# Kernel optimization log

Hardware: AMD Instinct MI355X
Metric: run time of the kernel (lower is better)

Reference implementation:

```python
import jax, jax.numpy as jnp
import numpy as np

INPUT_SIZE = 4
SEQ = 256
EMB = 64
QKV = 64
BATCH = 64
INDICES = np.array([0, 0, 1, 1])
BLK = SEQ // INPUT_SIZE                      # 64 positions per block
POS_GROUP = np.repeat(INDICES, BLK)          # per-position group id, shape [SEQ]
NUM_HEADS = len(np.unique(INDICES))          # 2
GROUP_POS = [np.where(POS_GROUP == g)[0] for g in range(NUM_HEADS)]  # static index sets


def _linear_params(key, din, dout):
    # torch nn.Linear default init: U(-1/sqrt(din), 1/sqrt(din))
    kw, kb = jax.random.split(key)
    s = 1.0 / np.sqrt(din)
    W = jax.random.uniform(kw, (dout, din), jnp.float32, -s, s)
    b = jax.random.uniform(kb, (dout,), jnp.float32, -s, s)
    return W, b


def setup_inputs() -> dict:
    key = jax.random.key(0)
    keys = jax.random.split(key, 1 + 3 * NUM_HEADS)
    inp = {"x": jax.random.normal(keys[0], (BATCH, SEQ, EMB), jnp.float32)}
    for g in range(NUM_HEADS):
        L = len(GROUP_POS[g])                # 128
        din, dout = L * EMB, L * QKV         # 8192 -> 8192
        WQ, bQ = _linear_params(keys[1 + 3 * g + 0], din, dout)
        WK, bK = _linear_params(keys[1 + 3 * g + 1], din, dout)
        WV, bV = _linear_params(keys[1 + 3 * g + 2], din, dout)
        inp[f"WQ{g}"], inp[f"bQ{g}"] = WQ, bQ
        inp[f"WK{g}"], inp[f"bK{g}"] = WK, bK
        inp[f"WV{g}"], inp[f"bV{g}"] = WV, bV
    return inp


def _head(xs, WQ, bQ, WK, bK, WV, bV, L):
    # xs: [B, L*EMB] flattened group slice
    B = xs.shape[0]
    Q = (xs @ WQ.T + bQ).reshape(B, L, QKV)
    K = (xs @ WK.T + bK).reshape(B, L, QKV)
    V = (xs @ WV.T + bV).reshape(B, L, QKV)
    scores = jnp.einsum("bik,bjk->bij", Q, K)        # [B, L, L]
    # Original uses nn.Softmax(dim=1): normalize over the QUERY axis (axis=1).
    attn = jax.nn.softmax(scores, axis=1)
    Z = jnp.einsum("bij,bjk->bik", attn, V)
    # coeff applied AFTER attention @ V, as in the original
    return Z * (1.0 / jnp.sqrt(jnp.float32(QKV)))


def reference(x, WQ0, bQ0, WK0, bK0, WV0, bV0, WQ1, bQ1, WK1, bK1, WV1, bV1):
    params = [(WQ0, bQ0, WK0, bK0, WV0, bV0), (WQ1, bQ1, WK1, bK1, WV1, bV1)]
    B = x.shape[0]
    out = jnp.zeros((B, SEQ, QKV), jnp.float32)
    for g in range(NUM_HEADS):                        # small static loop over groups
        pos = GROUP_POS[g]
        L = len(pos)
        xs = x[:, pos, :].reshape(B, L * EMB)
        Z = _head(xs, *params[g], L)
        out = out.at[:, pos, :].set(Z)
    return out
```

## Files before the change

### kernel.cpp

```cpp
#include <hip/hip_runtime.h>
#include <hip/hip_bf16.h>

#define BATCH 64
#define SEQ   256
#define EMB   64
#define QKVD  64
#define KD    8192
#define ND    8192
#define SEQD  16384
#define BKT   256
#define NTK   (KD / BKT)

typedef __attribute__((ext_vector_type(8))) short bf16x8;
typedef __attribute__((ext_vector_type(4))) float f32x4;

struct WArgs { const float* W[6]; const float* b[6]; };

__device__ __forceinline__ short f2bf(float f) {
    unsigned u = __builtin_bit_cast(unsigned, f);
    u += 0x7fffu + ((u >> 16) & 1u);
    return (short)(u >> 16);
}

__device__ __forceinline__ void gl16(const void* g, void* l) {
    __builtin_amdgcn_global_load_lds(
        (const __attribute__((address_space(1))) void*)g,
        (__attribute__((address_space(3))) void*)l, 16, 0, 0);
}

__device__ __forceinline__ void barrier_fenced() {
    asm volatile("" ::: "memory");
    __builtin_amdgcn_s_barrier();
    asm volatile("" ::: "memory");
}

__global__ __launch_bounds__(256)
void cvt_x_kernel(const float* __restrict__ x, short* __restrict__ xb) {
    const int i = (blockIdx.x * 256 + threadIdx.x) * 4;
    float4 v = *reinterpret_cast<const float4*>(x + i);
    short4 o;
    o.x = f2bf(v.x); o.y = f2bf(v.y); o.z = f2bf(v.z); o.w = f2bf(v.w);
    *reinterpret_cast<short4*>(xb + i) = o;
}

__global__ __launch_bounds__(256, 1)
void qkv_gemm_kernel(const short* __restrict__ xb, WArgs wa,
                     float* __restrict__ qkv) {
    __shared__ __attribute__((aligned(16))) float W_lds[2][64 * BKT];
    __shared__ __attribute__((aligned(16))) short A_lds[64 * BKT];

    const int wv = threadIdx.x >> 6;
    const int ln = threadIdx.x & 63;
    const int r  = ln & 15;
    const int kb = ln >> 4;
    const int key = r & 7;

    for (int nt = 0; nt < 3; ++nt) {
        const int logical = blockIdx.x * 3 + nt;
        const int gi = logical >> 7;
        const int n0 = (logical & 127) * 64;
        const int g  = gi / 3;

        const char*  __restrict__ Wb8 =
            (const char*)(wa.W[gi] + (size_t)(n0 + wv * 16) * KD);
        const short* __restrict__ Ag = xb + g * KD;

        f32x4 acc0 = {0.f, 0.f, 0.f, 0.f};
        f32x4 acc1 = acc0, acc2 = acc0, acc3 = acc0;

        auto stageW = [&](int t, int slot) {
            const char* tb = Wb8 + (size_t)t * 1024;
            #pragma unroll
            for (int i = 0; i < 16; ++i) {
                gl16(tb + (size_t)i * (KD * 4) + ((ln ^ (i & 7)) << 4),
                     (char*)&W_lds[slot][0] + (wv * 16 + i) * 1024);
            }
        };
        auto stageA = [&](int t) {
            #pragma unroll
            for (int j = 0; j < 8; ++j) {
                const int jj  = wv * 8 + j;
                const int row = 2 * jj + (ln >> 5);
                const int c   = (ln & 31) ^ (row & 7);
                gl16((const char*)(Ag + (size_t)row * SEQD) + (size_t)t * 512 + (c << 4),
                     (char*)&A_lds[0] + jj * 1024);
            }
        };

        auto compute = [&](int slot) {
            const float* Wrow = &W_lds[slot][0] + (wv * 16 + r) * BKT;
            const char*  Ab   = (const char*)&A_lds[0];
            #pragma unroll
            for (int s = 0; s < 8; ++s) {
                const int cg = s * 8 + kb * 2;
                f32x4 w0 = *(const f32x4*)(Wrow + (((cg)     ^ key) << 2));
                f32x4 w1 = *(const f32x4*)(Wrow + (((cg + 1) ^ key) << 2));
                bf16x8 bb;
                bb[0] = f2bf(w0[0]); bb[1] = f2bf(w0[1]);
                bb[2] = f2bf(w0[2]); bb[3] = f2bf(w0[3]);
                bb[4] = f2bf(w1[0]); bb[5] = f2bf(w1[1]);
                bb[6] = f2bf(w1[2]); bb[7] = f2bf(w1[3]);
                const int ca = (s * 4 + kb) ^ key;
                const bf16x8 a0 = *(const bf16x8*)(Ab + (r)      * 512 + (ca << 4));
                const bf16x8 a1 = *(const bf16x8*)(Ab + (r + 16) * 512 + (ca << 4));
                const bf16x8 a2 = *(const bf16x8*)(Ab + (r + 32) * 512 + (ca << 4));
                const bf16x8 a3 = *(const bf16x8*)(Ab + (r + 48) * 512 + (ca << 4));
                acc0 = __builtin_amdgcn_mfma_f32_16x16x32_bf16(a0, bb, acc0, 0, 0, 0);
                acc1 = __builtin_amdgcn_mfma_f32_16x16x32_bf16(a1, bb, acc1, 0, 0, 0);
                acc2 = __builtin_amdgcn_mfma_f32_16x16x32_bf16(a2, bb, acc2, 0, 0, 0);
                acc3 = __builtin_amdgcn_mfma_f32_16x16x32_bf16(a3, bb, acc3, 0, 0, 0);
            }
        };

        stageW(0, 0);
        stageA(0);
        stageW(1, 1);

        for (int t = 0; t < NTK; ++t) {
            if (t < NTK - 2) { asm volatile("s_waitcnt vmcnt(16)" ::: "memory"); }
            else             { asm volatile("s_waitcnt vmcnt(0)"  ::: "memory"); }
            __builtin_amdgcn_sched_barrier(0);
            barrier_fenced();
            compute(t & 1);
            barrier_fenced();
            if (t + 1 < NTK) stageA(t + 1);
            if (t + 2 < NTK) stageW(t + 2, t & 1);
        }
        barrier_fenced();

        const int nbr = n0 + wv * 16 + r;
        const float bias = wa.b[gi][nbr];
        float* orow = qkv + (size_t)gi * (BATCH * ND) + nbr;
        #pragma unroll
        for (int reg = 0; reg < 4; ++reg) {
            const int m = kb * 4 + reg;
            orow[(size_t)(m)      * ND] = acc0[reg] + bias;
            orow[(size_t)(m + 16) * ND] = acc1[reg] + bias;
            orow[(size_t)(m + 32) * ND] = acc2[reg] + bias;
            orow[(size_t)(m + 48) * ND] = acc3[reg] + bias;
        }
    }
}

__global__ __launch_bounds__(256)
void attn_kernel(const float* __restrict__ qkv, float* __restrict__ out) {
    __shared__ float Ql[128 * 65];
    __shared__ float Kl[128 * 65];
    __shared__ float Sc[128 * 129];
    __shared__ float Pm[256];
    __shared__ float Ps[256];
    __shared__ float Rden[128];

    const int b = blockIdx.x;
    const int g = blockIdx.y;
    const int t = threadIdx.x;

    const float* __restrict__ Qg = qkv + ((size_t)(3 * g + 0) * BATCH + b) * ND;
    const float* __restrict__ Kg = qkv + ((size_t)(3 * g + 1) * BATCH + b) * ND;
    const float* __restrict__ Vg = qkv + ((size_t)(3 * g + 2) * BATCH + b) * ND;

    for (int e = t; e < 8192; e += 256) {
        const int i = e >> 6, k = e & 63;
        Ql[i * 65 + k] = Qg[e];
        Kl[i * 65 + k] = Kg[e];
    }
    __syncthreads();

    {
        const int i0 = (t >> 4) * 8;
        const int j0 = (t & 15) * 8;
        float s[8][8];
        #pragma unroll
        for (int rr = 0; rr < 8; ++rr)
            #pragma unroll
            for (int cc = 0; cc < 8; ++cc) s[rr][cc] = 0.f;
        for (int k = 0; k < 64; ++k) {
            float qv[8], kv[8];
            #pragma unroll
            for (int rr = 0; rr < 8; ++rr) qv[rr] = Ql[(i0 + rr) * 65 + k];
            #pragma unroll
            for (int cc = 0; cc < 8; ++cc) kv[cc] = Kl[(j0 + cc) * 65 + k];
            #pragma unroll
            for (int rr = 0; rr < 8; ++rr)
                #pragma unroll
                for (int cc = 0; cc < 8; ++cc)
                    s[rr][cc] = fmaf(qv[rr], kv[cc], s[rr][cc]);
        }
        #pragma unroll
        for (int rr = 0; rr < 8; ++rr)
            #pragma unroll
            for (int cc = 0; cc < 8; ++cc)
                Sc[(i0 + rr) * 129 + (j0 + cc)] = s[rr][cc];
    }
    __syncthreads();

    const int j = t & 127, h = t >> 7;
    {
        for (int e = t; e < 8192; e += 256) {
            const int i = e >> 6, k = e & 63;
            Ql[i * 65 + k] = Vg[e];
        }
        float m = -3.0e38f;
        for (int i = h * 64; i < h * 64 + 64; ++i)
            m = fmaxf(m, Sc[i * 129 + j]);
        Pm[h * 128 + j] = m;
    }
    __syncthreads();
    {
        const float m = fmaxf(Pm[j], Pm[128 + j]);
        float sum = 0.f;
        for (int i = h * 64; i < h * 64 + 64; ++i) {
            const float e = __expf(Sc[i * 129 + j] - m);
            Sc[i * 129 + j] = e;
            sum += e;
        }
        Ps[h * 128 + j] = sum;
    }
    __syncthreads();
    if (t < 128) Rden[t] = 1.0f / (Ps[t] + Ps[128 + t]);
    __syncthreads();

    {
        const int i0 = (t >> 4) * 8;
        const int k0 = (t & 15) * 4;
        float z[8][4];
        #pragma unroll
        for (int rr = 0; rr < 8; ++rr)
            #pragma unroll
            for (int cc = 0; cc < 4; ++cc) z[rr][cc] = 0.f;
        for (int jj = 0; jj < 128; ++jj) {
            const float rd = Rden[jj];
            float av[8], vv[4];
            #pragma unroll
            for (int rr = 0; rr < 8; ++rr) av[rr] = Sc[(i0 + rr) * 129 + jj] * rd;
            #pragma unroll
            for (int cc = 0; cc < 4; ++cc) vv[cc] = Ql[jj * 65 + k0 + cc];
            #pragma unroll
            for (int rr = 0; rr < 8; ++rr)
                #pragma unroll
                for (int cc = 0; cc < 4; ++cc)
                    z[rr][cc] = fmaf(av[rr], vv[cc], z[rr][cc]);
        }
        float* op = out + (size_t)b * (SEQ * QKVD) + (size_t)(g * 128) * QKVD + k0;
        #pragma unroll
        for (int rr = 0; rr < 8; ++rr) {
            float4 o;
            o.x = z[rr][0] * 0.125f; o.y = z[rr][1] * 0.125f;
            o.z = z[rr][2] * 0.125f; o.w = z[rr][3] * 0.125f;
            *reinterpret_cast<float4*>(op + (size_t)(i0 + rr) * QKVD) = o;
        }
    }
}

extern "C" void kernel_launch(void* const* d_in, const int* in_sizes, int n_in,
                              void* d_out, int out_size, void* d_ws, size_t ws_size,
                              hipStream_t stream) {
    const float* x = (const float*)d_in[0];
    WArgs wa;
    for (int g = 0; g < 2; ++g)
        for (int q = 0; q < 3; ++q) {
            wa.W[g * 3 + q] = (const float*)d_in[1 + g * 6 + q * 2];
            wa.b[g * 3 + q] = (const float*)d_in[2 + g * 6 + q * 2];
        }

    short* xb  = (short*)d_ws;
    float* qkv = (float*)((char*)d_ws + (size_t)4 * 1024 * 1024);

    cvt_x_kernel<<<dim3(1024), dim3(256), 0, stream>>>(x, xb);
    qkv_gemm_kernel<<<dim3(256), dim3(256), 0, stream>>>(xb, wa, qkv);
    attn_kernel<<<dim3(BATCH, 2), dim3(256), 0, stream>>>(qkv, (float*)d_out);
}
```

Before: 345.0 us.

## Retile QKV GEMM to 32-column tiles with finer K pipelining and XCD-aware mapping

The QKV GEMM changes from 256 persistent blocks, each looping over three 64-column tiles, to 1536 blocks that each own one 32-column tile. Each wave now computes half the batch rows, with a deeper pipeline that double-buffers 512-wide W chunks and 128-wide A chunks. A block-index remap interleaves blocks across the 8 XCDs. The goal is better occupancy and overlap of the weight stream. The cost is that A is reloaded more often per weight byte, and the vmcnt bookkeeping is more complex.

New measurement: 515.9 us. 49.6% more time.

```diff
diff --git a/kernel.cpp b/kernel.cpp
--- a/kernel.cpp
+++ b/kernel.cpp
@@ -8,8 +8,10 @@
 #define KD    8192
 #define ND    8192
 #define SEQD  16384
-#define BKT   256
-#define NTK   (KD / BKT)
+#define BKP   512
+#define BKH2  128
+#define NPAIR (KD / BKP)
+#define NHALF (KD / BKH2)
 
 typedef __attribute__((ext_vector_type(8))) short bf16x8;
 typedef __attribute__((ext_vector_type(4))) float f32x4;
@@ -46,99 +48,127 @@
 __global__ __launch_bounds__(256, 1)
 void qkv_gemm_kernel(const short* __restrict__ xb, WArgs wa,
                      float* __restrict__ qkv) {
-    __shared__ __attribute__((aligned(16))) float W_lds[2][64 * BKT];
-    __shared__ __attribute__((aligned(16))) short A_lds[64 * BKT];
+    __shared__ __attribute__((aligned(16))) float W_lds[2][2][16 * BKP];
+    __shared__ __attribute__((aligned(16))) short A_lds[2][64 * BKH2];
 
     const int wv = threadIdx.x >> 6;
     const int ln = threadIdx.x & 63;
     const int r  = ln & 15;
     const int kb = ln >> 4;
-    const int key = r & 7;
-
-    for (int nt = 0; nt < 3; ++nt) {
-        const int logical = blockIdx.x * 3 + nt;
-        const int gi = logical >> 7;
-        const int n0 = (logical & 127) * 64;
-        const int g  = gi / 3;
-
-        const char*  __restrict__ Wb8 =
-            (const char*)(wa.W[gi] + (size_t)(n0 + wv * 16) * KD);
-        const short* __restrict__ Ag = xb + g * KD;
-
-        f32x4 acc0 = {0.f, 0.f, 0.f, 0.f};
-        f32x4 acc1 = acc0, acc2 = acc0, acc3 = acc0;
-
-        auto stageW = [&](int t, int slot) {
-            const char* tb = Wb8 + (size_t)t * 1024;
-            #pragma unroll
-            for (int i = 0; i < 16; ++i) {
-                gl16(tb + (size_t)i * (KD * 4) + ((ln ^ (i & 7)) << 4),
-                     (char*)&W_lds[slot][0] + (wv * 16 + i) * 1024);
+    const int gr = wv >> 1;
+    const int mh = wv & 1;
+
+    const int bid     = blockIdx.x;
+    const int logical = (bid & 7) * 192 + (bid >> 3);
+    const int gi      = logical >> 8;
+    const int n0      = (logical & 255) * 32;
+    const int g       = gi / 3;
+
+    const char*  __restrict__ Wgrp =
+        (const char*)(wa.W[gi] + (size_t)(n0 + gr * 16) * KD);
+    const short* __restrict__ Ag = xb + g * KD;
+
+    f32x4 acc0 = {0.f, 0.f, 0.f, 0.f};
+    f32x4 acc1 = acc0;
+
+    auto stageW = [&](int p, int slot) {
+        const char* pb = Wgrp + (size_t)p * 2048;
+        #pragma unroll
+        for (int i = 0; i < 8; ++i) {
+            const int row = mh * 8 + i;
+            const char* rp = pb + (size_t)row * (KD * 4);
+            char* ld = (char*)&W_lds[gr][slot][0] + row * 2048;
+            #pragma unroll
+            for (int j = 0; j < 2; ++j) {
+                const int sc = (j * 64 + ln) ^ (row & 7);
+                gl16(rp + sc * 16, ld + j * 1024 + ln * 16);
             }
-        };
-        auto stageA = [&](int t) {
-            #pragma unroll
-            for (int j = 0; j < 8; ++j) {
-                const int jj  = wv * 8 + j;
-                const int row = 2 * jj + (ln >> 5);
-                const int c   = (ln & 31) ^ (row & 7);
-                gl16((const char*)(Ag + (size_t)row * SEQD) + (size_t)t * 512 + (c << 4),
-                     (char*)&A_lds[0] + jj * 1024);
-            }
-        };
-
-        auto compute = [&](int slot) {
-            const float* Wrow = &W_lds[slot][0] + (wv * 16 + r) * BKT;
-            const char*  Ab   = (const char*)&A_lds[0];
-            #pragma unroll
-            for (int s = 0; s < 8; ++s) {
-                const int cg = s * 8 + kb * 2;
-                f32x4 w0 = *(const f32x4*)(Wrow + (((cg)     ^ key) << 2));
-                f32x4 w1 = *(const f32x4*)(Wrow + (((cg + 1) ^ key) << 2));
-                bf16x8 bb;
-                bb[0] = f2bf(w0[0]); bb[1] = f2bf(w0[1]);
-                bb[2] = f2bf(w0[2]); bb[3] = f2bf(w0[3]);
-                bb[4] = f2bf(w1[0]); bb[5] = f2bf(w1[1]);
-                bb[6] = f2bf(w1[2]); bb[7] = f2bf(w1[3]);
-                const int ca = (s * 4 + kb) ^ key;
-                const bf16x8 a0 = *(const bf16x8*)(Ab + (r)      * 512 + (ca << 4));
-                const bf16x8 a1 = *(const bf16x8*)(Ab + (r + 16) * 512 + (ca << 4));
-                const bf16x8 a2 = *(const bf16x8*)(Ab + (r + 32) * 512 + (ca << 4));
-                const bf16x8 a3 = *(const bf16x8*)(Ab + (r + 48) * 512 + (ca << 4));
-                acc0 = __builtin_amdgcn_mfma_f32_16x16x32_bf16(a0, bb, acc0, 0, 0, 0);
-                acc1 = __builtin_amdgcn_mfma_f32_16x16x32_bf16(a1, bb, acc1, 0, 0, 0);
-                acc2 = __builtin_amdgcn_mfma_f32_16x16x32_bf16(a2, bb, acc2, 0, 0, 0);
-                acc3 = __builtin_amdgcn_mfma_f32_16x16x32_bf16(a3, bb, acc3, 0, 0, 0);
-            }
-        };
-
-        stageW(0, 0);
-        stageA(0);
-        stageW(1, 1);
-
-        for (int t = 0; t < NTK; ++t) {
-            if (t < NTK - 2) { asm volatile("s_waitcnt vmcnt(16)" ::: "memory"); }
-            else             { asm volatile("s_waitcnt vmcnt(0)"  ::: "memory"); }
-            __builtin_amdgcn_sched_barrier(0);
-            barrier_fenced();
-            compute(t & 1);
-            barrier_fenced();
-            if (t + 1 < NTK) stageA(t + 1);
-            if (t + 2 < NTK) stageW(t + 2, t & 1);
-        }
-        barrier_fenced();
-
-        const int nbr = n0 + wv * 16 + r;
-        const float bias = wa.b[gi][nbr];
-        float* orow = qkv + (size_t)gi * (BATCH * ND) + nbr;
-        #pragma unroll
-        for (int reg = 0; reg < 4; ++reg) {
-            const int m = kb * 4 + reg;
-            orow[(size_t)(m)      * ND] = acc0[reg] + bias;
-            orow[(size_t)(m + 16) * ND] = acc1[reg] + bias;
-            orow[(size_t)(m + 32) * ND] = acc2[reg] + bias;
-            orow[(size_t)(m + 48) * ND] = acc3[reg] + bias;
-        }
+        }
+    };
+
+    auto stageA = [&](int h) {
+        short* slot = &A_lds[h & 1][0];
+        const char* hb = (const char*)Ag + (size_t)h * 256;
+        #pragma unroll
+        for (int ii = 0; ii < 4; ++ii) {
+            const int row = wv * 16 + ii * 4 + (ln >> 4);
+            const int sc  = (ln & 15) ^ ((row & 7) << 1);
+            gl16(hb + (size_t)row * (SEQD * 2) + sc * 16,
+                 (char*)slot + (wv * 4 + ii) * 1024 + ln * 16);
+        }
+    };
+
+    auto compute = [&](int h) {
+        const float* Wrow = &W_lds[gr][(h >> 2) & 1][0] + r * BKP;
+        const char*  Ab   = (const char*)&A_lds[h & 1][0];
+        const int    key  = r & 7;
+        #pragma unroll
+        for (int s = 0; s < 4; ++s) {
+            const int lg = (h & 3) * 32 + s * 8 + kb * 2;
+            f32x4 w0 = *(const f32x4*)(Wrow + (((lg)     ^ key) << 2));
+            f32x4 w1 = *(const f32x4*)(Wrow + (((lg + 1) ^ key) << 2));
+            bf16x8 bb;
+            bb[0] = f2bf(w0[0]); bb[1] = f2bf(w0[1]);
+            bb[2] = f2bf(w0[2]); bb[3] = f2bf(w0[3]);
+            bb[4] = f2bf(w1[0]); bb[5] = f2bf(w1[1]);
+            bb[6] = f2bf(w1[2]); bb[7] = f2bf(w1[3]);
+            const int ca = ((s * 4 + kb) ^ (key << 1)) << 4;
+            const bf16x8 a0 = *(const bf16x8*)(Ab + (mh * 32 + r)      * 256 + ca);
+            const bf16x8 a1 = *(const bf16x8*)(Ab + (mh * 32 + 16 + r) * 256 + ca);
+            acc0 = __builtin_amdgcn_mfma_f32_16x16x32_bf16(a0, bb, acc0, 0, 0, 0);
+            acc1 = __builtin_amdgcn_mfma_f32_16x16x32_bf16(a1, bb, acc1, 0, 0, 0);
+        }
+    };
+
+    stageW(0, 0);
+    stageA(0);
+    stageA(1);
+    __builtin_amdgcn_sched_barrier(0);
+
+    for (int p = 0; p < NPAIR; ++p) {
+        const int h = 4 * p;
+        const bool morew = (p + 1 < NPAIR);
+
+        asm volatile("s_waitcnt vmcnt(4)" ::: "memory");
+        barrier_fenced();
+        compute(h);
+        barrier_fenced();
+        stageA(h + 2);
+        __builtin_amdgcn_sched_barrier(0);
+
+        asm volatile("s_waitcnt vmcnt(4)" ::: "memory");
+        barrier_fenced();
+        compute(h + 1);
+        barrier_fenced();
+        stageA(h + 3);
+        if (morew) stageW(p + 1, (p + 1) & 1);
+        __builtin_amdgcn_sched_barrier(0);
+
+        if (morew) { asm volatile("s_waitcnt vmcnt(20)" ::: "memory"); }
+        else       { asm volatile("s_waitcnt vmcnt(4)"  ::: "memory"); }
+        barrier_fenced();
+        compute(h + 2);
+        barrier_fenced();
+        if (h + 4 < NHALF) stageA(h + 4);
+        __builtin_amdgcn_sched_barrier(0);
+
+        if (morew) { asm volatile("s_waitcnt vmcnt(20)" ::: "memory"); }
+        else       { asm volatile("s_waitcnt vmcnt(0)"  ::: "memory"); }
+        barrier_fenced();
+        compute(h + 3);
+        barrier_fenced();
+        if (h + 5 < NHALF) stageA(h + 5);
+        __builtin_amdgcn_sched_barrier(0);
+    }
+
+    const int nbr = n0 + gr * 16 + r;
+    const float bias = wa.b[gi][nbr];
+    float* orow = qkv + (size_t)gi * (BATCH * ND) + nbr;
+    #pragma unroll
+    for (int reg = 0; reg < 4; ++reg) {
+        const int m = mh * 32 + kb * 4 + reg;
+        orow[(size_t)(m)      * ND] = acc0[reg] + bias;
+        orow[(size_t)(m + 16) * ND] = acc1[reg] + bias;
     }
 }
 
@@ -267,6 +297,6 @@
     float* qkv = (float*)((char*)d_ws + (size_t)4 * 1024 * 1024);
 
     cvt_x_kernel<<<dim3(1024), dim3(256), 0, stream>>>(x, xb);
-    qkv_gemm_kernel<<<dim3(256), dim3(256), 0, stream>>>(xb, wa, qkv);
+    qkv_gemm_kernel<<<dim3(1536), dim3(256), 0, stream>>>(xb, wa, qkv);
     attn_kernel<<<dim3(BATCH, 2), dim3(256), 0, stream>>>(qkv, (float*)d_out);
 }
```

## Split QKV GEMM into smaller 32x32 tiles over many XCD-mapped blocks

Applied to the files above, without the earlier changes.

The QKV projection GEMM moves from 256 persistent blocks, each looping over three 64-column tiles, to 3072 blocks. Each block computes a 32x32 output tile, with the batch dimension split in two halves. Block IDs are remapped so the two M-halves that share a weight tile land on the same XCD, meaning the second read of those fp32 weights should hit L2. Two blocks per CU plus smaller LDS buffers aim to raise occupancy and keep more memory requests in flight on this weight-bandwidth-bound kernel. The cost is that each weight tile is now loaded twice, plus more block launch overhead.

Measured after the change: 401.6 us. 16.4% more time.

```diff
diff --git a/kernel.cpp b/kernel.cpp
--- a/kernel.cpp
+++ b/kernel.cpp
@@ -43,102 +43,98 @@
     *reinterpret_cast<short4*>(xb + i) = o;
 }
 
-__global__ __launch_bounds__(256, 1)
+__global__ __launch_bounds__(256, 2)
 void qkv_gemm_kernel(const short* __restrict__ xb, WArgs wa,
                      float* __restrict__ qkv) {
-    __shared__ __attribute__((aligned(16))) float W_lds[2][64 * BKT];
-    __shared__ __attribute__((aligned(16))) short A_lds[64 * BKT];
-
-    const int wv = threadIdx.x >> 6;
-    const int ln = threadIdx.x & 63;
-    const int r  = ln & 15;
-    const int kb = ln >> 4;
+    __shared__ __attribute__((aligned(16))) float W_lds[2][32 * BKT];
+    __shared__ __attribute__((aligned(16))) short A_lds[32 * BKT];
+
+    const int wv  = threadIdx.x >> 6;
+    const int ln  = threadIdx.x & 63;
+    const int r   = ln & 15;
+    const int kb  = ln >> 4;
     const int key = r & 7;
-
-    for (int nt = 0; nt < 3; ++nt) {
-        const int logical = blockIdx.x * 3 + nt;
-        const int gi = logical >> 7;
-        const int n0 = (logical & 127) * 64;
-        const int g  = gi / 3;
-
-        const char*  __restrict__ Wb8 =
-            (const char*)(wa.W[gi] + (size_t)(n0 + wv * 16) * KD);
-        const short* __restrict__ Ag = xb + g * KD;
-
-        f32x4 acc0 = {0.f, 0.f, 0.f, 0.f};
-        f32x4 acc1 = acc0, acc2 = acc0, acc3 = acc0;
-
-        auto stageW = [&](int t, int slot) {
-            const char* tb = Wb8 + (size_t)t * 1024;
-            #pragma unroll
-            for (int i = 0; i < 16; ++i) {
-                gl16(tb + (size_t)i * (KD * 4) + ((ln ^ (i & 7)) << 4),
-                     (char*)&W_lds[slot][0] + (wv * 16 + i) * 1024);
-            }
-        };
-        auto stageA = [&](int t) {
-            #pragma unroll
-            for (int j = 0; j < 8; ++j) {
-                const int jj  = wv * 8 + j;
-                const int row = 2 * jj + (ln >> 5);
-                const int c   = (ln & 31) ^ (row & 7);
-                gl16((const char*)(Ag + (size_t)row * SEQD) + (size_t)t * 512 + (c << 4),
-                     (char*)&A_lds[0] + jj * 1024);
-            }
-        };
-
-        auto compute = [&](int slot) {
-            const float* Wrow = &W_lds[slot][0] + (wv * 16 + r) * BKT;
-            const char*  Ab   = (const char*)&A_lds[0];
-            #pragma unroll
-            for (int s = 0; s < 8; ++s) {
-                const int cg = s * 8 + kb * 2;
-                f32x4 w0 = *(const f32x4*)(Wrow + (((cg)     ^ key) << 2));
-                f32x4 w1 = *(const f32x4*)(Wrow + (((cg + 1) ^ key) << 2));
-                bf16x8 bb;
-                bb[0] = f2bf(w0[0]); bb[1] = f2bf(w0[1]);
-                bb[2] = f2bf(w0[2]); bb[3] = f2bf(w0[3]);
-                bb[4] = f2bf(w1[0]); bb[5] = f2bf(w1[1]);
-                bb[6] = f2bf(w1[2]); bb[7] = f2bf(w1[3]);
-                const int ca = (s * 4 + kb) ^ key;
-                const bf16x8 a0 = *(const bf16x8*)(Ab + (r)      * 512 + (ca << 4));
-                const bf16x8 a1 = *(const bf16x8*)(Ab + (r + 16) * 512 + (ca << 4));
-                const bf16x8 a2 = *(const bf16x8*)(Ab + (r + 32) * 512 + (ca << 4));
-                const bf16x8 a3 = *(const bf16x8*)(Ab + (r + 48) * 512 + (ca << 4));
-                acc0 = __builtin_amdgcn_mfma_f32_16x16x32_bf16(a0, bb, acc0, 0, 0, 0);
-                acc1 = __builtin_amdgcn_mfma_f32_16x16x32_bf16(a1, bb, acc1, 0, 0, 0);
-                acc2 = __builtin_amdgcn_mfma_f32_16x16x32_bf16(a2, bb, acc2, 0, 0, 0);
-                acc3 = __builtin_amdgcn_mfma_f32_16x16x32_bf16(a3, bb, acc3, 0, 0, 0);
-            }
-        };
-
-        stageW(0, 0);
-        stageA(0);
-        stageW(1, 1);
-
-        for (int t = 0; t < NTK; ++t) {
-            if (t < NTK - 2) { asm volatile("s_waitcnt vmcnt(16)" ::: "memory"); }
-            else             { asm volatile("s_waitcnt vmcnt(0)"  ::: "memory"); }
-            __builtin_amdgcn_sched_barrier(0);
-            barrier_fenced();
-            compute(t & 1);
-            barrier_fenced();
-            if (t + 1 < NTK) stageA(t + 1);
-            if (t + 2 < NTK) stageW(t + 2, t & 1);
-        }
+    const int mq  = wv & 1;
+    const int nq  = wv >> 1;
+
+    const int bid = blockIdx.x;
+    const int xcd = bid & 7;
+    const int q   = bid >> 3;
+    const int mh  = q & 1;
+    const int p   = xcd * 192 + (q >> 1);
+    const int gi  = p >> 8;
+    const int n0  = (p & 255) * 32;
+    const int g   = gi / 3;
+    const int m0  = mh * 32;
+
+    const char*  __restrict__ Wb8 =
+        (const char*)(wa.W[gi] + (size_t)n0 * KD);
+    const short* __restrict__ Ag = xb + g * KD;
+
+    f32x4 acc = {0.f, 0.f, 0.f, 0.f};
+
+    auto stageW = [&](int t, int slot) {
+        const char* tb = Wb8 + (size_t)t * 1024;
+        #pragma unroll
+        for (int i = 0; i < 8; ++i) {
+            const int row = wv * 8 + i;
+            gl16(tb + (size_t)row * (KD * 4) + ((ln ^ (row & 7)) << 4),
+                 (char*)&W_lds[slot][0] + row * 1024);
+        }
+    };
+    auto stageA = [&](int t) {
+        #pragma unroll
+        for (int j = 0; j < 4; ++j) {
+            const int jj  = wv * 4 + j;
+            const int row = 2 * jj + (ln >> 5);
+            const int c   = (ln & 31) ^ (row & 7);
+            gl16((const char*)(Ag + (size_t)(m0 + row) * SEQD)
+                     + (size_t)t * 512 + (c << 4),
+                 (char*)&A_lds[0] + jj * 1024);
+        }
+    };
+
+    auto compute = [&](int slot) {
+        const float* Wrow = &W_lds[slot][0] + (nq * 16 + r) * BKT;
+        const char*  Ab   = (const char*)&A_lds[0] + (mq * 16 + r) * 512;
+        #pragma unroll
+        for (int s = 0; s < 8; ++s) {
+            const int cg = s * 8 + kb * 2;
+            f32x4 w0 = *(const f32x4*)(Wrow + (((cg)     ^ key) << 2));
+            f32x4 w1 = *(const f32x4*)(Wrow + (((cg + 1) ^ key) << 2));
+            bf16x8 bb;
+            bb[0] = f2bf(w0[0]); bb[1] = f2bf(w0[1]);
+            bb[2] = f2bf(w0[2]); bb[3] = f2bf(w0[3]);
+            bb[4] = f2bf(w1[0]); bb[5] = f2bf(w1[1]);
+            bb[6] = f2bf(w1[2]); bb[7] = f2bf(w1[3]);
+            const int ca = (s * 4 + kb) ^ key;
+            const bf16x8 a = *(const bf16x8*)(Ab + (ca << 4));
+            acc = __builtin_amdgcn_mfma_f32_16x16x32_bf16(a, bb, acc, 0, 0, 0);
+        }
+    };
+
+    stageW(0, 0);
+    stageA(0);
+    stageW(1, 1);
+
+    for (int t = 0; t < NTK; ++t) {
+        if (t < NTK - 1) { asm volatile("s_waitcnt vmcnt(8)" ::: "memory"); }
+        else             { asm volatile("s_waitcnt vmcnt(0)" ::: "memory"); }
+        __builtin_amdgcn_sched_barrier(0);
         barrier_fenced();
-
-        const int nbr = n0 + wv * 16 + r;
-        const float bias = wa.b[gi][nbr];
-        float* orow = qkv + (size_t)gi * (BATCH * ND) + nbr;
-        #pragma unroll
-        for (int reg = 0; reg < 4; ++reg) {
-            const int m = kb * 4 + reg;
-            orow[(size_t)(m)      * ND] = acc0[reg] + bias;
-            orow[(size_t)(m + 16) * ND] = acc1[reg] + bias;
-            orow[(size_t)(m + 32) * ND] = acc2[reg] + bias;
-            orow[(size_t)(m + 48) * ND] = acc3[reg] + bias;
-        }
+        compute(t & 1);
+        barrier_fenced();
+        if (t + 1 < NTK) stageA(t + 1);
+        if (t + 2 < NTK) stageW(t + 2, t & 1);
+    }
+
+    const int nbr = n0 + nq * 16 + r;
+    const float bias = wa.b[gi][nbr];
+    float* orow = qkv + (size_t)gi * (BATCH * ND) + nbr;
+    #pragma unroll
+    for (int reg = 0; reg < 4; ++reg) {
+        const int m = m0 + mq * 16 + kb * 4 + reg;
+        orow[(size_t)m * ND] = acc[reg] + bias;
     }
 }
 
@@ -267,6 +263,6 @@
     float* qkv = (float*)((char*)d_ws + (size_t)4 * 1024 * 1024);
 
     cvt_x_kernel<<<dim3(1024), dim3(256), 0, stream>>>(x, xb);
-    qkv_gemm_kernel<<<dim3(256), dim3(256), 0, stream>>>(xb, wa, qkv);
+    qkv_gemm_kernel<<<dim3(3072), dim3(256), 0, stream>>>(xb, wa, qkv);
     attn_kernel<<<dim3(BATCH, 2), dim3(256), 0, stream>>>(qkv, (float*)d_out);
 }
```
